# Kernel optimization log

Measured on AMD Instinct MI355X. Metric: run time of the kernel, lower is better.

## Reference

```python
import jax, jax.numpy as jnp
import numpy as np

HIDDEN = 5120
N_HEADS = 16           # 128 total heads / DEVICE_NUM=8
Q_LORA = 1536
KV_LORA = 512
NOPE = 128
ROPE = 64
QK_DIM = NOPE + ROPE   # 192
V_DIM = 128
EPS = 1e-6
ROPE_BASE = 10000.0
SCALE_BY_DEVICE = 1.0 / 8.0
SOFTMAX_SCALE = QK_DIM ** -0.5
B, S = 1, 2048


def rms_norm(x, w, eps=EPS):
    v = jnp.mean(jnp.square(x), axis=-1, keepdims=True)
    return x * jax.lax.rsqrt(v + eps) * w


def rotate_half(x):
    h = x.shape[-1] // 2
    return jnp.concatenate([-x[..., h:], x[..., :h]], axis=-1)


def interleave(x):
    # DeepSeek rope layout: view(b,h,s,d//2,2).transpose(-1,-2).reshape(b,h,s,d)
    b, h, s, d = x.shape
    return jnp.swapaxes(x.reshape(b, h, s, d // 2, 2), -1, -2).reshape(b, h, s, d)


def setup_inputs() -> dict:
    key = jax.random.key(0)
    ks = jax.random.split(key, 8)
    w = 0.02
    hidden_states = jax.random.normal(ks[0], (B, S, HIDDEN), dtype=jnp.float32)
    position_ids = jnp.arange(S, dtype=jnp.int64 if jax.config.jax_enable_x64 else jnp.int32)[None, :]
    causal = jnp.tril(jnp.ones((S, S), dtype=bool))
    attention_mask = jnp.where(causal, 0.0, -1e9).astype(jnp.float32)[None, None]
    return {
        'hidden_states': hidden_states,
        'position_ids': position_ids,
        'attention_mask': attention_mask,
        'ln_w': jnp.ones((HIDDEN,), jnp.float32),
        'wq_a': jax.random.normal(ks[1], (Q_LORA, HIDDEN), jnp.float32) * w,
        'q_a_ln_w': jnp.ones((Q_LORA,), jnp.float32),
        'wq_b': jax.random.normal(ks[2], (N_HEADS * QK_DIM, Q_LORA), jnp.float32) * w,
        'wkv_a': jax.random.normal(ks[3], (KV_LORA + ROPE, HIDDEN), jnp.float32) * w,
        'kv_a_ln_w': jnp.ones((KV_LORA,), jnp.float32),
        'wkv_b': jax.random.normal(ks[4], (N_HEADS * (NOPE + V_DIM), KV_LORA), jnp.float32) * w,
        'wo': jax.random.normal(ks[5], (HIDDEN, N_HEADS * V_DIM), jnp.float32) * w,
    }


def reference(hidden_states, position_ids, attention_mask, ln_w, wq_a, q_a_ln_w,
              wq_b, wkv_a, kv_a_ln_w, wkv_b, wo):
    b, s, _ = hidden_states.shape
    residual = hidden_states * SCALE_BY_DEVICE
    h = rms_norm(hidden_states, ln_w)

    # Q low-rank decompression: q_a_proj -> RMSNorm -> q_b_proj
    q = rms_norm(h @ wq_a.T, q_a_ln_w) @ wq_b.T
    q = q.reshape(b, s, N_HEADS, QK_DIM).transpose(0, 2, 1, 3)  # b,h,s,192
    q_nope, q_pe = q[..., :NOPE], q[..., NOPE:]

    # KV low-rank: kv_a_proj_with_mqa -> split -> RMSNorm -> kv_b_proj
    ckv = h @ wkv_a.T                                           # b,s,512+64
    c_kv, k_pe = ckv[..., :KV_LORA], ckv[..., KV_LORA:]
    k_pe = k_pe[:, None, :, :]                                  # b,1,s,64
    kv = rms_norm(c_kv, kv_a_ln_w) @ wkv_b.T
    kv = kv.reshape(b, s, N_HEADS, NOPE + V_DIM).transpose(0, 2, 1, 3)
    k_nope, v = kv[..., :NOPE], kv[..., NOPE:]

    # RoPE (DeepSeek interleaved layout)
    inv_freq = 1.0 / (ROPE_BASE ** (jnp.arange(0, ROPE, 2, dtype=jnp.float32) / ROPE))
    freqs = position_ids.astype(jnp.float32)[..., None] * inv_freq  # b,s,32
    emb = jnp.concatenate([freqs, freqs], axis=-1)                  # b,s,64
    cos = jnp.cos(emb)[:, None]                                     # b,1,s,64
    sin = jnp.sin(emb)[:, None]
    q_pe = interleave(q_pe)
    k_pe = interleave(k_pe)
    q_pe = q_pe * cos + rotate_half(q_pe) * sin
    k_pe = k_pe * cos + rotate_half(k_pe) * sin

    k = jnp.concatenate([k_nope, jnp.broadcast_to(k_pe, (b, N_HEADS, s, ROPE))], axis=-1)
    qf = jnp.concatenate([q_nope, q_pe], axis=-1)

    scores = jnp.einsum('bhqd,bhkd->bhqk', qf, k) * SOFTMAX_SCALE + attention_mask
    attn = jax.nn.softmax(scores.astype(jnp.float32), axis=-1).astype(qf.dtype)
    out = jnp.einsum('bhqk,bhkd->bhqd', attn, v)                    # b,h,s,128
    out = out.transpose(0, 2, 1, 3).reshape(b, s, N_HEADS * V_DIM) @ wo.T

    hidden_states = residual + out
    return (hidden_states.astype(jnp.float32), k.astype(jnp.float32), v.astype(jnp.float32))
```

## Files before the change

kernel.cpp:

```cpp
#include <hip/hip_runtime.h>
#include <hip/hip_bf16.h>

typedef __hip_bfloat16 bf16;
typedef __attribute__((ext_vector_type(8))) short bf16x8;
typedef __attribute__((ext_vector_type(4))) float f32x4;

#define S_LEN   2048
#define HIDDEN  5120
#define NHEADS  16
#define QLORA   1536
#define KVLORA  512
#define QKD     192
#define VD      128
#define QN      (NHEADS*QKD)
#define KVN     (NHEADS*(128+VD))
#define QCKN    2112
#define SM_SCALE 0.07216878364870322f

__device__ __forceinline__ f32x4 mfma16(bf16x8 a, bf16x8 b, f32x4 c) {
  return __builtin_amdgcn_mfma_f32_16x16x32_bf16(a, b, c, 0, 0, 0);
}
__device__ __forceinline__ void g2l16(const void* g, void* l) {
  __builtin_amdgcn_global_load_lds((const __attribute__((address_space(1))) void*)g,
                                   (__attribute__((address_space(3))) void*)l, 16, 0, 0);
}
__device__ __forceinline__ bf16x8 ld8(const bf16* p) { return *(const bf16x8*)p; }

__global__ void init_k(float4* __restrict__ qa_ckv, int n_qa,
                       float4* __restrict__ q_f, int n_q,
                       const float4* __restrict__ hs, float4* __restrict__ oh, int n_h)
{
  int i = blockIdx.x * 256 + threadIdx.x;
  if (i < n_qa) { qa_ckv[i] = (float4){0.f, 0.f, 0.f, 0.f}; return; }
  if ((i -= n_qa) < n_q) { q_f[i] = (float4){0.f, 0.f, 0.f, 0.f}; return; }
  if ((i -= n_q) < n_h) {
    float4 v = hs[i];
    v.x *= 0.125f; v.y *= 0.125f; v.z *= 0.125f; v.w *= 0.125f;
    oh[i] = v;
  }
}

__global__ void cvt_multi(const float* s0, bf16* d0, int n0,
                          const float* s1, bf16* d1, int n1,
                          const float* s2, bf16* d2, int n2,
                          const float* s3, bf16* d3, int n3,
                          const float* s4, bf16* d4, int n4s)
{
  int i = blockIdx.x * 256 + threadIdx.x;
  const float* s; bf16* d;
  if (i < n0) { s = s0; d = d0; }
  else if ((i -= n0) < n1) { s = s1; d = d1; }
  else if ((i -= n1) < n2) { s = s2; d = d2; }
  else if ((i -= n2) < n3) { s = s3; d = d3; }
  else if ((i -= n3) < n4s) { s = s4; d = d4; }
  else return;
  const float4 v = ((const float4*)s)[i];
  union { bf16 b[4]; unsigned long long u; } pk;
  pk.b[0] = __float2bfloat16(v.x);
  pk.b[1] = __float2bfloat16(v.y);
  pk.b[2] = __float2bfloat16(v.z);
  pk.b[3] = __float2bfloat16(v.w);
  *(unsigned long long*)(d + (size_t)i * 4) = pk.u;
}

__global__ void rmsnorm_k(const float* __restrict__ in, int istride, int C,
                          const float* __restrict__ w,
                          bf16* __restrict__ out, int ostride)
{
  const int row = blockIdx.x;
  const float* x = in + (size_t)row * istride;
  float ss = 0.f;
  for (int c = threadIdx.x; c < C; c += 256) { float v = x[c]; ss += v * v; }
  #pragma unroll
  for (int m = 32; m >= 1; m >>= 1) ss += __shfl_xor(ss, m, 64);
  __shared__ float red[4];
  if ((threadIdx.x & 63) == 0) red[threadIdx.x >> 6] = ss;
  __syncthreads();
  ss = red[0] + red[1] + red[2] + red[3];
  const float sc = rsqrtf(ss / (float)C + 1e-6f);
  bf16* o = out + (size_t)row * ostride;
  for (int c = threadIdx.x; c < C; c += 256)
    o[c] = __float2bfloat16(x[c] * sc * w[c]);
}

template<bool CLAMPN, bool ATOMIC>
__global__ __launch_bounds__(256, 2)
void gemm_nt(const bf16* __restrict__ A, const bf16* __restrict__ Bt,
             float* __restrict__ C, int M, int N, int lda, int klen)
{
  __shared__ bf16 As[2 * 128 * 32];
  __shared__ bf16 Bs[2 * 128 * 32];
  const int tid = threadIdx.x;
  const int wave = tid >> 6;
  const int lane = tid & 63;
  const int l15 = lane & 15, quad = lane >> 4;
  const int bm = blockIdx.x * 128, bn = blockIdx.y * 128;
  const int kbase = blockIdx.z * klen;
  const int wm = (wave >> 1) * 64, wn = (wave & 1) * 64;

  const int srow = tid >> 2;
  const int scol = (tid & 3) * 8;
  const bf16* Ag0 = A + (size_t)(bm + srow) * lda + kbase + scol;
  const bf16* Ag1 = A + (size_t)(bm + 64 + srow) * lda + kbase + scol;
  int bn0 = bn + srow, bn1 = bn + 64 + srow;
  if (CLAMPN) { bn0 = min(bn0, N - 1); bn1 = min(bn1, N - 1); }
  const bf16* Bg0 = Bt + (size_t)bn0 * lda + kbase + scol;
  const bf16* Bg1 = Bt + (size_t)bn1 * lda + kbase + scol;

  char* AsW = (char*)As + wave * 1024;
  char* BsW = (char*)Bs + wave * 1024;

  f32x4 acc[4][4];
  #pragma unroll
  for (int i = 0; i < 4; i++)
    #pragma unroll
    for (int j = 0; j < 4; j++) acc[i][j] = (f32x4){0.f, 0.f, 0.f, 0.f};

  const int nk = klen >> 6;
  for (int kt = 0; kt < nk; ++kt) {
    const int k0 = kt << 6;
    #pragma unroll
    for (int c = 0; c < 2; ++c) {
      g2l16(Ag0 + k0 + c * 32, AsW + c * 8192);
      g2l16(Ag1 + k0 + c * 32, AsW + c * 8192 + 4096);
      g2l16(Bg0 + k0 + c * 32, BsW + c * 8192);
      g2l16(Bg1 + k0 + c * 32, BsW + c * 8192 + 4096);
    }
    __syncthreads();
    #pragma unroll
    for (int c = 0; c < 2; ++c) {
      bf16x8 af[4], bfr[4];
      #pragma unroll
      for (int i = 0; i < 4; i++)
        af[i] = ld8(As + c * 4096 + (wm + i * 16 + l15) * 32 + quad * 8);
      #pragma unroll
      for (int j = 0; j < 4; j++)
        bfr[j] = ld8(Bs + c * 4096 + (wn + j * 16 + l15) * 32 + quad * 8);
      #pragma unroll
      for (int i = 0; i < 4; i++)
        #pragma unroll
        for (int j = 0; j < 4; j++)
          acc[i][j] = mfma16(af[i], bfr[j], acc[i][j]);
    }
    __syncthreads();
  }

  #pragma unroll
  for (int i = 0; i < 4; i++)
    #pragma unroll
    for (int j = 0; j < 4; j++) {
      const int row = bm + wm + i * 16 + quad * 4;
      const int col = bn + wn + j * 16 + l15;
      if (!CLAMPN || col < N) {
        #pragma unroll
        for (int r = 0; r < 4; r++) {
          const float v = acc[i][j][r];
          const size_t idx = (size_t)(row + r) * N + col;
          if (ATOMIC) unsafeAtomicAdd(&C[idx], v);
          else        C[idx] = v;
        }
      }
    }
}

__global__ void rope_assemble_k(
    const float* __restrict__ q,
    const float* __restrict__ qackv,
    const float* __restrict__ kv,
    const int*   __restrict__ pos,
    float* __restrict__ k_out,
    bf16*  __restrict__ q_bf,
    bf16*  __restrict__ k_bf)
{
  const int s = blockIdx.x;
  const int t = threadIdx.x;
  __shared__ float cs[32], sn[32], kpe[64];
  const float p = (float)pos[s];
  if (t < 32) {
    const float inv = powf(10000.0f, -((float)(2 * t)) / 64.0f);
    const float f = p * inv;
    float si, c;
    sincosf(f, &si, &c);
    cs[t] = c; sn[t] = si;
    const float r0v = qackv[(size_t)s * QCKN + 2048 + 2 * t];
    const float r1v = qackv[(size_t)s * QCKN + 2048 + 2 * t + 1];
    kpe[t]      = r0v * c - r1v * si;
    kpe[32 + t] = r1v * c + r0v * si;
  }
  __syncthreads();
  for (int i = t; i < NHEADS * 128; i += 256) {
    const int h = i >> 7, d = i & 127;
    const size_t o = ((size_t)h * S_LEN + s) * QKD + d;
    const float kn = kv[(size_t)s * KVN + h * 256 + d];
    k_out[o] = kn;
    k_bf[o] = __float2bfloat16(kn);
    q_bf[o] = __float2bfloat16(q[(size_t)s * QN + h * QKD + d]);
  }
  for (int i = t; i < NHEADS * 32; i += 256) {
    const int h = i >> 5, jj = i & 31;
    const float r0v = q[(size_t)s * QN + h * QKD + 128 + 2 * jj];
    const float r1v = q[(size_t)s * QN + h * QKD + 128 + 2 * jj + 1];
    const float c = cs[jj], si = sn[jj];
    const size_t o = ((size_t)h * S_LEN + s) * QKD + 128;
    q_bf[o + jj]      = __float2bfloat16(r0v * c - r1v * si);
    q_bf[o + 32 + jj] = __float2bfloat16(r1v * c + r0v * si);
  }
  for (int i = t; i < NHEADS * 64; i += 256) {
    const int h = i >> 6, jj = i & 63;
    const float v = kpe[jj];
    const size_t o = ((size_t)h * S_LEN + s) * QKD + 128 + jj;
    k_out[o] = v;
    k_bf[o] = __float2bfloat16(v);
  }
}

__global__ void v_transpose_k(const float* __restrict__ kv,
                              float* __restrict__ v_out,
                              bf16* __restrict__ vt_bf)
{
  const int h = blockIdx.x, st = blockIdx.y, dt = blockIdx.z;
  __shared__ float tile[32][33];
  const int tx = threadIdx.x & 31;
  const int ty = (threadIdx.x >> 5) * 4;
  const int s0 = st * 32, d0 = dt * 32;
  #pragma unroll
  for (int r = 0; r < 4; r++) {
    const int sl = ty + r;
    const float v = kv[(size_t)(s0 + sl) * KVN + h * 256 + 128 + d0 + tx];
    v_out[((size_t)h * S_LEN + s0 + sl) * VD + d0 + tx] = v;
    tile[sl][tx] = v;
  }
  __syncthreads();
  #pragma unroll
  for (int r = 0; r < 4; r++) {
    const int dl = ty + r;
    vt_bf[((size_t)h * VD + d0 + dl) * S_LEN + s0 + tx] = __float2bfloat16(tile[tx][dl]);
  }
}

__global__ __launch_bounds__(256, 3)
void attn_k(const bf16* __restrict__ qb, const bf16* __restrict__ kb,
            const bf16* __restrict__ vt, bf16* __restrict__ aout)
{
  const int head = blockIdx.y;
  const int qt = (head < 8) ? blockIdx.x : (gridDim.x - 1 - blockIdx.x);
  const int wave = threadIdx.x >> 6, lane = threadIdx.x & 63;
  const int l15 = lane & 15, quad = lane >> 4;
  const int r0 = qt * 64 + wave * 16;

  const bf16* qh = qb + (size_t)head * S_LEN * QKD;
  const bf16* kh = kb + (size_t)head * S_LEN * QKD;
  const bf16* vh = vt + (size_t)head * VD * S_LEN;

  __shared__ bf16 Ks[6 * 64 * 32];
  __shared__ bf16 Vs[128 * 72];
  __shared__ bf16 Plds[4][16][72];

  const int tid = threadIdx.x;
  const int srow = wave * 16 + (lane >> 2);
  const int scol = (lane & 3) * 8;
  const bf16* ksrc = kh + (size_t)srow * QKD + scol;
  bf16* kdst = Ks + srow * 32 + scol;
  const int vrow = tid >> 1;
  const int vcol = (tid & 1) * 32;
  const bf16* vsrc = vh + (size_t)vrow * S_LEN + vcol;
  bf16* vdst = Vs + vrow * 72 + vcol;

  bf16x8 qf[6];
  #pragma unroll
  for (int c = 0; c < 6; ++c)
    qf[c] = ld8(qh + (size_t)(r0 + l15) * QKD + c * 32 + quad * 8);

  f32x4 O[8];
  #pragma unroll
  for (int d = 0; d < 8; ++d) O[d] = (f32x4){0.f, 0.f, 0.f, 0.f};
  float mrow[4] = {-1e30f, -1e30f, -1e30f, -1e30f};
  float lrow[4] = {0.f, 0.f, 0.f, 0.f};

  bf16x8 kreg[6], vreg[4];
  #pragma unroll
  for (int c = 0; c < 6; ++c) kreg[c] = ld8(ksrc + c * 32);
  #pragma unroll
  for (int c = 0; c < 4; ++c) vreg[c] = ld8(vsrc + c * 8);

  for (int j = 0; j <= qt; ++j) {
    __syncthreads();
    #pragma unroll
    for (int c = 0; c < 6; ++c) *(bf16x8*)(kdst + c * 2048) = kreg[c];
    #pragma unroll
    for (int c = 0; c < 4; ++c) *(bf16x8*)(vdst + c * 8) = vreg[c];
    __syncthreads();
    if (j < qt) {
      const bf16* src = ksrc + (size_t)(j + 1) * 64 * QKD;
      #pragma unroll
      for (int c = 0; c < 6; ++c) kreg[c] = ld8(src + c * 32);
      const bf16* vs2 = vsrc + (size_t)(j + 1) * 64;
      #pragma unroll
      for (int c = 0; c < 4; ++c) vreg[c] = ld8(vs2 + c * 8);
    }
    const int kc = j * 64;

    f32x4 S[4];
    #pragma unroll
    for (int nt = 0; nt < 4; ++nt) S[nt] = (f32x4){0.f, 0.f, 0.f, 0.f};
    #pragma unroll
    for (int c = 0; c < 6; ++c) {
      #pragma unroll
      for (int nt = 0; nt < 4; ++nt) {
        const bf16x8 kf = ld8(Ks + c * 2048 + (nt * 16 + l15) * 32 + quad * 8);
        S[nt] = mfma16(qf[c], kf, S[nt]);
      }
    }

    float mnew[4] = {-1e30f, -1e30f, -1e30f, -1e30f};
    if (j == qt) {
      #pragma unroll
      for (int nt = 0; nt < 4; ++nt) {
        const int col = kc + nt * 16 + l15;
        #pragma unroll
        for (int r = 0; r < 4; r++) {
          const int row = r0 + quad * 4 + r;
          const float v = (col <= row) ? S[nt][r] * SM_SCALE : -1e30f;
          S[nt][r] = v;
          mnew[r] = fmaxf(mnew[r], v);
        }
      }
    } else {
      #pragma unroll
      for (int nt = 0; nt < 4; ++nt)
        #pragma unroll
        for (int r = 0; r < 4; r++) {
          const float v = S[nt][r] * SM_SCALE;
          S[nt][r] = v;
          mnew[r] = fmaxf(mnew[r], v);
        }
    }
    #pragma unroll
    for (int m = 8; m >= 1; m >>= 1)
      #pragma unroll
      for (int r = 0; r < 4; r++)
        mnew[r] = fmaxf(mnew[r], __shfl_xor(mnew[r], m, 64));
    float alpha[4], ladd[4] = {0.f, 0.f, 0.f, 0.f};
    #pragma unroll
    for (int r = 0; r < 4; r++) {
      const float mi = fmaxf(mrow[r], mnew[r]);
      alpha[r] = __expf(mrow[r] - mi);
      mrow[r] = mi;
    }
    #pragma unroll
    for (int nt = 0; nt < 4; ++nt)
      #pragma unroll
      for (int r = 0; r < 4; r++) {
        const float pv = __expf(S[nt][r] - mrow[r]);
        S[nt][r] = pv;
        ladd[r] += pv;
      }
    #pragma unroll
    for (int m = 8; m >= 1; m >>= 1)
      #pragma unroll
      for (int r = 0; r < 4; r++) ladd[r] += __shfl_xor(ladd[r], m, 64);
    #pragma unroll
    for (int r = 0; r < 4; r++) lrow[r] = lrow[r] * alpha[r] + ladd[r];
    #pragma unroll
    for (int d = 0; d < 8; ++d)
      #pragma unroll
      for (int r = 0; r < 4; r++) O[d][r] *= alpha[r];

    #pragma unroll
    for (int nt = 0; nt < 4; ++nt)
      #pragma unroll
      for (int r = 0; r < 4; r++)
        Plds[wave][quad * 4 + r][nt * 16 + l15] = __float2bfloat16(S[nt][r]);

    #pragma unroll
    for (int kt = 0; kt < 2; ++kt) {
      const bf16x8 pf = ld8(&Plds[wave][l15][kt * 32 + quad * 8]);
      #pragma unroll
      for (int dt = 0; dt < 8; ++dt) {
        const bf16x8 vf = ld8(Vs + (dt * 16 + l15) * 72 + kt * 32 + quad * 8);
        O[dt] = mfma16(pf, vf, O[dt]);
      }
    }
  }

  #pragma unroll
  for (int dt = 0; dt < 8; ++dt) {
    const int col = head * VD + dt * 16 + l15;
    #pragma unroll
    for (int r = 0; r < 4; r++) {
      const int row = r0 + quad * 4 + r;
      aout[(size_t)row * (NHEADS * VD) + col] = __float2bfloat16(O[dt][r] / lrow[r]);
    }
  }
}

extern "C" void kernel_launch(void* const* d_in, const int* in_sizes, int n_in,
                              void* d_out, int out_size, void* d_ws, size_t ws_size,
                              hipStream_t stream)
{
  const float* hs      = (const float*)d_in[0];
  const int*   pos     = (const int*)  d_in[1];
  const float* ln_w    = (const float*)d_in[3];
  const float* wq_a    = (const float*)d_in[4];
  const float* q_a_ln  = (const float*)d_in[5];
  const float* wq_b    = (const float*)d_in[6];
  const float* wkv_a   = (const float*)d_in[7];
  const float* kv_a_ln = (const float*)d_in[8];
  const float* wkv_b   = (const float*)d_in[9];
  const float* wo      = (const float*)d_in[10];

  float* out_hidden = (float*)d_out;
  float* out_k = out_hidden + (size_t)S_LEN * HIDDEN;
  float* out_v = out_k + (size_t)NHEADS * S_LEN * QKD;

  char* ws = (char*)d_ws;
  size_t off = 0;
  auto alloc = [&](size_t bytes) { char* p = ws + off; off += (bytes + 255) & ~255ULL; return p; };

  bf16* h_b     = (bf16*)alloc((size_t)S_LEN * HIDDEN * 2);
  bf16* w1_b    = (bf16*)alloc((size_t)QCKN * HIDDEN * 2);
  bf16* wqb_b   = (bf16*)alloc((size_t)QN * QLORA * 2);
  bf16* wkvb_b  = (bf16*)alloc((size_t)KVN * KVLORA * 2);
  bf16* wo_b    = (bf16*)alloc((size_t)HIDDEN * (NHEADS * VD) * 2);
  float* qa_ckv = (float*)alloc((size_t)S_LEN * QCKN * 4);
  float* q_f    = (float*)alloc((size_t)S_LEN * QN * 4);
  bf16* qa_n    = (bf16*)alloc((size_t)S_LEN * QLORA * 2);
  bf16* ckv_n   = (bf16*)alloc((size_t)S_LEN * KVLORA * 2);
  float* kv_f   = (float*)alloc((size_t)S_LEN * KVN * 4);
  bf16* q_bf    = (bf16*)alloc((size_t)NHEADS * S_LEN * QKD * 2);
  bf16* k_bf    = (bf16*)alloc((size_t)NHEADS * S_LEN * QKD * 2);
  bf16* vt_bf   = (bf16*)alloc((size_t)NHEADS * VD * S_LEN * 2);
  bf16* attn_b  = (bf16*)alloc((size_t)S_LEN * (NHEADS * VD) * 2);

  {
    const int n_qa = (int)((size_t)S_LEN * QCKN / 4);
    const int n_q  = (int)((size_t)S_LEN * QN / 4);
    const int n_h  = (int)((size_t)S_LEN * HIDDEN / 4);
    const int tot = n_qa + n_q + n_h;
    init_k<<<(tot + 255) / 256, 256, 0, stream>>>(
        (float4*)qa_ckv, n_qa, (float4*)q_f, n_q,
        (const float4*)hs, (float4*)out_hidden, n_h);
  }

  {
    const int n0 = (QLORA * HIDDEN) / 4;
    const int n1 = ((QCKN - QLORA) * HIDDEN) / 4;
    const int n2 = (QN * QLORA) / 4;
    const int n3 = (KVN * KVLORA) / 4;
    const int n4s = (HIDDEN * NHEADS * VD) / 4;
    const int tot = n0 + n1 + n2 + n3 + n4s;
    cvt_multi<<<(tot + 255) / 256, 256, 0, stream>>>(
        wq_a, w1_b, n0,
        wkv_a, w1_b + (size_t)QLORA * HIDDEN, n1,
        wq_b, wqb_b, n2,
        wkv_b, wkvb_b, n3,
        wo, wo_b, n4s);
  }

  rmsnorm_k<<<S_LEN, 256, 0, stream>>>(hs, HIDDEN, HIDDEN, ln_w, h_b, HIDDEN);

  gemm_nt<true, true><<<dim3(16, 17, 4), 256, 0, stream>>>(
      h_b, w1_b, qa_ckv, S_LEN, QCKN, HIDDEN, HIDDEN / 4);

  rmsnorm_k<<<S_LEN, 256, 0, stream>>>(qa_ckv, QCKN, QLORA, q_a_ln, qa_n, QLORA);
  rmsnorm_k<<<S_LEN, 256, 0, stream>>>(qa_ckv + QLORA, QCKN, KVLORA, kv_a_ln, ckv_n, KVLORA);

  gemm_nt<false, true><<<dim3(16, QN / 128, 2), 256, 0, stream>>>(
      qa_n, wqb_b, q_f, S_LEN, QN, QLORA, QLORA / 2);
  gemm_nt<false, false><<<dim3(16, KVN / 128, 1), 256, 0, stream>>>(
      ckv_n, wkvb_b, kv_f, S_LEN, KVN, KVLORA, KVLORA);

  rope_assemble_k<<<S_LEN, 256, 0, stream>>>(q_f, qa_ckv, kv_f, pos, out_k, q_bf, k_bf);
  v_transpose_k<<<dim3(NHEADS, S_LEN / 32, VD / 32), 256, 0, stream>>>(kv_f, out_v, vt_bf);

  attn_k<<<dim3(S_LEN / 64, NHEADS), 256, 0, stream>>>(q_bf, k_bf, vt_bf, attn_b);

  gemm_nt<false, true><<<dim3(16, HIDDEN / 128, 2), 256, 0, stream>>>(
      attn_b, wo_b, out_hidden, S_LEN, HIDDEN, NHEADS * VD, (NHEADS * VD) / 2);

  (void)in_sizes; (void)n_in; (void)out_size; (void)ws_size;
}
```

Measured before the change: 627.6 us.

## Fuse residual into output GEMM, drop split-K, merge RMSNorms, raise occupancy

The residual scaling (hs*0.125) moves out of the init kernel and into the epilogue of the output-projection GEMM. That GEMM now runs without split-K and uses plain stores instead of atomics, which removes a full read and write pass over out_hidden and the atomic traffic. The two LoRA RMSNorm launches are merged into one kernel, and the GEMM launch bounds are raised to 4 blocks per CU. Dropping split-K halves the number of blocks in the output GEMM (16x40 = 640 blocks), which may hurt load balance. The higher occupancy target could also cause register spills.

```diff
diff --git a/kernel.cpp b/kernel.cpp
--- a/kernel.cpp
+++ b/kernel.cpp
@@ -27,17 +27,11 @@
 __device__ __forceinline__ bf16x8 ld8(const bf16* p) { return *(const bf16x8*)p; }
 
 __global__ void init_k(float4* __restrict__ qa_ckv, int n_qa,
-                       float4* __restrict__ q_f, int n_q,
-                       const float4* __restrict__ hs, float4* __restrict__ oh, int n_h)
+                       float4* __restrict__ q_f, int n_q)
 {
   int i = blockIdx.x * 256 + threadIdx.x;
   if (i < n_qa) { qa_ckv[i] = (float4){0.f, 0.f, 0.f, 0.f}; return; }
-  if ((i -= n_qa) < n_q) { q_f[i] = (float4){0.f, 0.f, 0.f, 0.f}; return; }
-  if ((i -= n_q) < n_h) {
-    float4 v = hs[i];
-    v.x *= 0.125f; v.y *= 0.125f; v.z *= 0.125f; v.w *= 0.125f;
-    oh[i] = v;
-  }
+  if ((i -= n_qa) < n_q) q_f[i] = (float4){0.f, 0.f, 0.f, 0.f};
 }
 
 __global__ void cvt_multi(const float* s0, bf16* d0, int n0,
@@ -83,10 +77,35 @@
     o[c] = __float2bfloat16(x[c] * sc * w[c]);
 }
 
-template<bool CLAMPN, bool ATOMIC>
-__global__ __launch_bounds__(256, 2)
+__global__ void rmsnorm2_k(const float* __restrict__ qackv,
+                           const float* __restrict__ wq, const float* __restrict__ wk,
+                           bf16* __restrict__ qa_n, bf16* __restrict__ ckv_n)
+{
+  const int r = blockIdx.x;
+  const bool is_q = r < S_LEN;
+  const int row = is_q ? r : r - S_LEN;
+  const int C = is_q ? QLORA : KVLORA;
+  const float* x = qackv + (size_t)row * QCKN + (is_q ? 0 : QLORA);
+  const float* w = is_q ? wq : wk;
+  bf16* o = (is_q ? qa_n + (size_t)row * QLORA : ckv_n + (size_t)row * KVLORA);
+  float ss = 0.f;
+  for (int c = threadIdx.x; c < C; c += 256) { float v = x[c]; ss += v * v; }
+  #pragma unroll
+  for (int m = 32; m >= 1; m >>= 1) ss += __shfl_xor(ss, m, 64);
+  __shared__ float red[4];
+  if ((threadIdx.x & 63) == 0) red[threadIdx.x >> 6] = ss;
+  __syncthreads();
+  ss = red[0] + red[1] + red[2] + red[3];
+  const float sc = rsqrtf(ss / (float)C + 1e-6f);
+  for (int c = threadIdx.x; c < C; c += 256)
+    o[c] = __float2bfloat16(x[c] * sc * w[c]);
+}
+
+template<bool RESID, bool CLAMPN, bool ATOMIC>
+__global__ __launch_bounds__(256, 4)
 void gemm_nt(const bf16* __restrict__ A, const bf16* __restrict__ Bt,
-             float* __restrict__ C, int M, int N, int lda, int klen)
+             float* __restrict__ C, int M, int N, int lda, int klen,
+             const float* __restrict__ resid, float rscale)
 {
   __shared__ bf16 As[2 * 128 * 32];
   __shared__ bf16 Bs[2 * 128 * 32];
@@ -154,8 +173,9 @@
       if (!CLAMPN || col < N) {
         #pragma unroll
         for (int r = 0; r < 4; r++) {
-          const float v = acc[i][j][r];
+          float v = acc[i][j][r];
           const size_t idx = (size_t)(row + r) * N + col;
+          if (RESID) v += resid[idx] * rscale;
           if (ATOMIC) unsafeAtomicAdd(&C[idx], v);
           else        C[idx] = v;
         }
@@ -435,11 +455,9 @@
   {
     const int n_qa = (int)((size_t)S_LEN * QCKN / 4);
     const int n_q  = (int)((size_t)S_LEN * QN / 4);
-    const int n_h  = (int)((size_t)S_LEN * HIDDEN / 4);
-    const int tot = n_qa + n_q + n_h;
+    const int tot = n_qa + n_q;
     init_k<<<(tot + 255) / 256, 256, 0, stream>>>(
-        (float4*)qa_ckv, n_qa, (float4*)q_f, n_q,
-        (const float4*)hs, (float4*)out_hidden, n_h);
+        (float4*)qa_ckv, n_qa, (float4*)q_f, n_q);
   }
 
   {
@@ -459,24 +477,23 @@
 
   rmsnorm_k<<<S_LEN, 256, 0, stream>>>(hs, HIDDEN, HIDDEN, ln_w, h_b, HIDDEN);
 
-  gemm_nt<true, true><<<dim3(16, 17, 4), 256, 0, stream>>>(
-      h_b, w1_b, qa_ckv, S_LEN, QCKN, HIDDEN, HIDDEN / 4);
-
-  rmsnorm_k<<<S_LEN, 256, 0, stream>>>(qa_ckv, QCKN, QLORA, q_a_ln, qa_n, QLORA);
-  rmsnorm_k<<<S_LEN, 256, 0, stream>>>(qa_ckv + QLORA, QCKN, KVLORA, kv_a_ln, ckv_n, KVLORA);
-
-  gemm_nt<false, true><<<dim3(16, QN / 128, 2), 256, 0, stream>>>(
-      qa_n, wqb_b, q_f, S_LEN, QN, QLORA, QLORA / 2);
-  gemm_nt<false, false><<<dim3(16, KVN / 128, 1), 256, 0, stream>>>(
-      ckv_n, wkvb_b, kv_f, S_LEN, KVN, KVLORA, KVLORA);
+  gemm_nt<false, true, true><<<dim3(16, 17, 4), 256, 0, stream>>>(
+      h_b, w1_b, qa_ckv, S_LEN, QCKN, HIDDEN, HIDDEN / 4, nullptr, 0.f);
+
+  rmsnorm2_k<<<2 * S_LEN, 256, 0, stream>>>(qa_ckv, q_a_ln, kv_a_ln, qa_n, ckv_n);
+
+  gemm_nt<false, false, true><<<dim3(16, QN / 128, 2), 256, 0, stream>>>(
+      qa_n, wqb_b, q_f, S_LEN, QN, QLORA, QLORA / 2, nullptr, 0.f);
+  gemm_nt<false, false, false><<<dim3(16, KVN / 128, 1), 256, 0, stream>>>(
+      ckv_n, wkvb_b, kv_f, S_LEN, KVN, KVLORA, KVLORA, nullptr, 0.f);
 
   rope_assemble_k<<<S_LEN, 256, 0, stream>>>(q_f, qa_ckv, kv_f, pos, out_k, q_bf, k_bf);
   v_transpose_k<<<dim3(NHEADS, S_LEN / 32, VD / 32), 256, 0, stream>>>(kv_f, out_v, vt_bf);
 
   attn_k<<<dim3(S_LEN / 64, NHEADS), 256, 0, stream>>>(q_bf, k_bf, vt_bf, attn_b);
 
-  gemm_nt<false, true><<<dim3(16, HIDDEN / 128, 2), 256, 0, stream>>>(
-      attn_b, wo_b, out_hidden, S_LEN, HIDDEN, NHEADS * VD, (NHEADS * VD) / 2);
+  gemm_nt<true, false, false><<<dim3(16, HIDDEN / 128, 1), 256, 0, stream>>>(
+      attn_b, wo_b, out_hidden, S_LEN, HIDDEN, NHEADS * VD, NHEADS * VD, hs, 0.125f);
 
   (void)in_sizes; (void)n_in; (void)out_size; (void)ws_size;
 }
```

After: 594.2 us. -5.3%, faster.
